# Optimization experiments

Measured on AMD Instinct MI355X. Metric: run time of the kernel, lower is better.

The kernel has to match this reference:

```python
import jax, jax.numpy as jnp
import numpy as np

D = 512       # input_embedding_dimensions
H = 2         # num_heads
HD = D // H   # head_dim = 256
B = 16
S = 1194      # max_sequence_length


def setup_inputs() -> dict:
    key = jax.random.key(0)
    k1, k2, k3, k4, k5 = jax.random.split(key, 5)
    scale_in = 1.0 / np.sqrt(D)
    return {
        "positional_embeddings": jax.random.normal(k1, (B, S, D), dtype=jnp.float32),
        "W_qkv": jax.random.uniform(k2, (D, 3 * D), minval=-scale_in, maxval=scale_in, dtype=jnp.float32),
        "b_qkv": jax.random.uniform(k3, (3 * D,), minval=-scale_in, maxval=scale_in, dtype=jnp.float32),
        "W_out": jax.random.uniform(k4, (D, D), minval=-scale_in, maxval=scale_in, dtype=jnp.float32),
        "b_out": jax.random.uniform(k5, (D,), minval=-scale_in, maxval=scale_in, dtype=jnp.float32),
    }


def reference(positional_embeddings, W_qkv, b_qkv, W_out, b_out):
    x = positional_embeddings              # [B, S, D]
    b, s, _ = x.shape
    qkv = x @ W_qkv + b_qkv                # [B, S, 3D]
    q, k, v = jnp.split(qkv, 3, axis=-1)

    def split_heads(t):
        return t.reshape(b, s, H, HD).transpose(0, 2, 1, 3)  # [B, H, S, HD]

    q, k, v = split_heads(q), split_heads(k), split_heads(v)
    scores = jnp.einsum("bhqd,bhkd->bhqk", q, k) / jnp.sqrt(jnp.float32(HD))
    causal = jnp.tril(jnp.ones((s, s), dtype=bool))          # [S, S]
    scores = jnp.where(causal[None, None, :, :], scores, -jnp.inf)
    att = jax.nn.softmax(scores, axis=-1)                    # [B, H, S, S]
    out = jnp.einsum("bhqk,bhkd->bhqd", att, v)              # [B, H, S, HD]
    out = out.transpose(0, 2, 1, 3).reshape(b, s, D)         # [B, S, D]
    return out @ W_out + b_out
```

## Files before the change

### kernel.cpp

```cpp
#include <hip/hip_runtime.h>
#include <stdint.h>

#define D_    512
#define H_    2
#define HD_   256
#define B_    16
#define S_    1194
#define MTOK  19104
#define MPAD  19200
#define SPAD  1216
#define NQKV  1536
#define NKT   38
#define LOG2E 1.44269504088896340736f

typedef unsigned short u16;
typedef __attribute__((ext_vector_type(8))) short bf16x8;
typedef __attribute__((ext_vector_type(4))) float f32x4;

__device__ inline u16 f2bf(float x) {
  union { float f; unsigned u; } c; c.f = x;
  unsigned r = c.u + 0x7fffu + ((c.u >> 16) & 1u);
  return (u16)(r >> 16);
}

__device__ inline void async_copy16(void* lds, const void* g) {
  __builtin_amdgcn_global_load_lds(
      (__attribute__((address_space(1))) void*)(g),
      (__attribute__((address_space(3))) void*)(lds),
      16, 0, 0);
}

__global__ void convert_kernel(const float* __restrict__ X,
                               const float* __restrict__ Wqkv,
                               const float* __restrict__ Wout,
                               u16* __restrict__ Xf,
                               u16* __restrict__ Wqf,
                               u16* __restrict__ Wof) {
  const int NXG = MPAD * 64;
  const int NQG = 12 * 8 * 16 * 64;
  const int NOG = 4 * 8 * 16 * 64;
  const int TOT = NXG + NQG + NOG;
  int stride = gridDim.x * blockDim.x;
  for (int g = blockIdx.x * blockDim.x + threadIdx.x; g < TOT; g += stride) {
    if (g < NXG) {
      int lane = g & 63, f = (g >> 6) & 15, kt = (g >> 10) & 7, mt = g >> 13;
      int i = mt * 128 + (f & 7) * 16 + (lane & 15);
      int k = kt * 64 + (f >> 3) * 32 + (lane >> 4) * 8;
      bf16x8 o;
      if (i < MTOK) {
        f32x4 v0 = *(const f32x4*)&X[(size_t)i * 512 + k];
        f32x4 v1 = *(const f32x4*)&X[(size_t)i * 512 + k + 4];
#pragma unroll
        for (int e = 0; e < 4; ++e) { o[e] = (short)f2bf(v0[e]); o[4 + e] = (short)f2bf(v1[e]); }
      } else {
#pragma unroll
        for (int e = 0; e < 8; ++e) o[e] = 0;
      }
      *(bf16x8*)&Xf[(size_t)g * 8] = o;
    } else if (g < NXG + NQG) {
      int gg = g - NXG;
      int lane = gg & 63, f = (gg >> 6) & 15, kt = (gg >> 10) & 7, nt = gg >> 13;
      int j = nt * 128 + (f & 7) * 16 + (lane & 15);
      int k = kt * 64 + (f >> 3) * 32 + (lane >> 4) * 8;
      bf16x8 o;
#pragma unroll
      for (int e = 0; e < 8; ++e) o[e] = (short)f2bf(Wqkv[(size_t)(k + e) * NQKV + j]);
      *(bf16x8*)&Wqf[(size_t)gg * 8] = o;
    } else {
      int gg = g - NXG - NQG;
      int lane = gg & 63, f = (gg >> 6) & 15, kt = (gg >> 10) & 7, nt = gg >> 13;
      int j = nt * 128 + (f & 7) * 16 + (lane & 15);
      int k = kt * 64 + (f >> 3) * 32 + (lane >> 4) * 8;
      bf16x8 o;
#pragma unroll
      for (int e = 0; e < 8; ++e) o[e] = (short)f2bf(Wout[(size_t)(k + e) * 512 + j]);
      *(bf16x8*)&Wof[(size_t)gg * 8] = o;
    }
  }
}

template<int MODE>
__global__ __launch_bounds__(256, 2) void gemm_kernel(
    const u16* __restrict__ Af, const u16* __restrict__ Bf,
    const float* __restrict__ bias, int nb,
    u16* __restrict__ Qb, u16* __restrict__ Kf, u16* __restrict__ Vf,
    float* __restrict__ Cout)
{
  __shared__ u16 ldsA[2][16 * 512];
  __shared__ u16 ldsB[2][16 * 512];

  const int t  = threadIdx.x;
  const int l  = t & 63;
  const int w  = t >> 6;
  const int lr = l >> 4, lc = l & 15;

  const int nwg = gridDim.x;
  const int qq = nwg >> 3, rr8 = nwg & 7;
  const int xcd = blockIdx.x & 7, off = blockIdx.x >> 3;
  const int wgid = (xcd < rr8 ? xcd * (qq + 1) : rr8 * (qq + 1) + (xcd - rr8) * qq) + off;
  const int m0 = (wgid / nb) * 128;
  const int n0 = (wgid % nb) * 128;

  const u16* pA = Af + ((size_t)(m0 >> 7) * 128 + w) * 512 + l * 8;
  const u16* pB = Bf + ((size_t)(n0 >> 7) * 128 + w) * 512 + l * 8;

  f32x4 acc[4][4] = {};

#pragma unroll
  for (int c = 0; c < 4; ++c) {
    async_copy16(&ldsA[0][(c * 4 + w) * 512], pA + c * 2048);
    async_copy16(&ldsB[0][(c * 4 + w) * 512], pB + c * 2048);
  }
  __syncthreads();

  for (int kt = 0; kt < 8; ++kt) {
    const int cur = kt & 1;
    if (kt < 7) {
      const u16* qA = pA + (kt + 1) * 8192;
      const u16* qB = pB + (kt + 1) * 8192;
#pragma unroll
      for (int c = 0; c < 4; ++c) {
        async_copy16(&ldsA[cur ^ 1][(c * 4 + w) * 512], qA + c * 2048);
        async_copy16(&ldsB[cur ^ 1][(c * 4 + w) * 512], qB + c * 2048);
      }
    }
#pragma unroll
    for (int kk = 0; kk < 2; ++kk) {
      bf16x8 af[4], bfr[4];
#pragma unroll
      for (int m = 0; m < 4; ++m)
        af[m] = *(bf16x8*)&ldsA[cur][((kk * 8 + (w >> 1) * 4 + m) * 64 + l) * 8];
#pragma unroll
      for (int n = 0; n < 4; ++n)
        bfr[n] = *(bf16x8*)&ldsB[cur][((kk * 8 + (w & 1) * 4 + n) * 64 + l) * 8];
      __builtin_amdgcn_s_setprio(1);
#pragma unroll
      for (int m = 0; m < 4; ++m)
#pragma unroll
        for (int n = 0; n < 4; ++n)
          acc[m][n] = __builtin_amdgcn_mfma_f32_16x16x32_bf16(af[m], bfr[n], acc[m][n], 0, 0, 0);
      __builtin_amdgcn_s_setprio(0);
    }
    __syncthreads();
  }

  int jv[4]; float bj[4];
#pragma unroll
  for (int n = 0; n < 4; ++n) { jv[n] = n0 + (w & 1) * 64 + n * 16 + lc; bj[n] = bias[jv[n]]; }

#pragma unroll
  for (int m = 0; m < 4; ++m) {
#pragma unroll
    for (int r = 0; r < 4; ++r) {
      int i = m0 + (w >> 1) * 64 + m * 16 + lr * 4 + r;
      if (i >= MTOK) continue;
      if (MODE == 0) {
        int b = i / S_, s = i - b * S_;
        int stK  = s >> 5;
        int nfs  = (s >> 4) & 1;
        int lisK = s & 15;
        int lvhi = (s >> 3) & 3;
        int es   = s & 7;
#pragma unroll
        for (int n = 0; n < 4; ++n) {
          int j = jv[n];
          int which = j >> 9, h = (j >> 8) & 1, d = j & 255;
          int bh = b * H_ + h;
          u16 v = f2bf(acc[m][n][r] + bj[n]);
          if (which == 0) {
            Qb[((size_t)(bh * SPAD + s)) * HD_ + d] = v;
          } else if (which == 1) {
            Kf[(((size_t)(bh * NKT + stK)) * 16 + (d >> 5) * 2 + nfs) * 512 +
               (((d >> 3) & 3) * 16 + lisK) * 8 + (d & 7)] = v;
          } else {
            Vf[(((size_t)(bh * NKT + stK)) * 16 + (d >> 4)) * 512 +
               (lvhi * 16 + (d & 15)) * 8 + es] = v;
          }
        }
      } else {
#pragma unroll
        for (int n = 0; n < 4; ++n)
          Cout[(size_t)i * D_ + jv[n]] = acc[m][n][r] + bj[n];
      }
    }
  }
}

__global__ __launch_bounds__(256, 2) void attn_kernel(
    const u16* __restrict__ Qb, const u16* __restrict__ Kf,
    const u16* __restrict__ Vf, u16* __restrict__ Obf)
{
  __shared__ u16 ldsK[2][16 * 512];
  __shared__ u16 ldsV[2][16 * 512];
  __shared__ u16 ldsP[4][16 * 36];

  const int id   = blockIdx.x;
  const int xcd  = id & 7;
  const int slot = id >> 3;
  const int bh   = xcd + 8 * (slot / 19);
  const int qt   = 18 - (slot % 19);
  const int q0   = qt * 64;
  const int nkv  = 2 * qt + 2;
  const int t  = threadIdx.x, l = t & 63, w = t >> 6;
  const int lr = l >> 4, lc = l & 15;
  const int wq0 = q0 + w * 16;

  bf16x8 qf[8];
  const u16* qbase = Qb + (size_t)(bh * SPAD + wq0 + lc) * HD_ + lr * 8;
#pragma unroll
  for (int kb = 0; kb < 8; ++kb)
    qf[kb] = *(const bf16x8*)(qbase + kb * 32);

  f32x4 oacc[16] = {};
  float mrow[4] = {-1e30f, -1e30f, -1e30f, -1e30f};
  float lsum[4] = {0.f, 0.f, 0.f, 0.f};

  {
    const u16* kb_ = Kf + (((size_t)(bh * NKT)) * 16 + w) * 512 + l * 8;
    const u16* vb_ = Vf + (((size_t)(bh * NKT)) * 16 + w) * 512 + l * 8;
#pragma unroll
    for (int c = 0; c < 4; ++c) {
      async_copy16(&ldsK[0][(c * 4 + w) * 512], kb_ + c * 2048);
      async_copy16(&ldsV[0][(c * 4 + w) * 512], vb_ + c * 2048);
    }
  }
  __syncthreads();

  for (int kt = 0; kt < nkv; ++kt) {
    const int cur = kt & 1;
    if (kt + 1 < nkv) {
      const u16* kb_ = Kf + (((size_t)(bh * NKT + kt + 1)) * 16 + w) * 512 + l * 8;
      const u16* vb_ = Vf + (((size_t)(bh * NKT + kt + 1)) * 16 + w) * 512 + l * 8;
#pragma unroll
      for (int c = 0; c < 4; ++c) {
        async_copy16(&ldsK[cur ^ 1][(c * 4 + w) * 512], kb_ + c * 2048);
        async_copy16(&ldsV[cur ^ 1][(c * 4 + w) * 512], vb_ + c * 2048);
      }
    }

    f32x4 sacc[2] = {};
    __builtin_amdgcn_s_setprio(1);
#pragma unroll
    for (int kb = 0; kb < 8; ++kb) {
#pragma unroll
      for (int nf = 0; nf < 2; ++nf) {
        bf16x8 kf = *(bf16x8*)&ldsK[cur][((kb * 2 + nf) * 64 + l) * 8];
        sacc[nf] = __builtin_amdgcn_mfma_f32_16x16x32_bf16(qf[kb], kf, sacc[nf], 0, 0, 0);
      }
    }
    __builtin_amdgcn_s_setprio(0);

    const int kv0 = kt * 32;
    float sval[2][4];
    float pm[4] = {-1e30f, -1e30f, -1e30f, -1e30f};
    if (kv0 + 31 <= wq0) {
#pragma unroll
      for (int nf = 0; nf < 2; ++nf)
#pragma unroll
        for (int r = 0; r < 4; ++r) {
          float v = sacc[nf][r] * 0.0625f;
          sval[nf][r] = v;
          pm[r] = fmaxf(pm[r], v);
        }
    } else {
#pragma unroll
      for (int nf = 0; nf < 2; ++nf) {
        int col = kv0 + nf * 16 + lc;
#pragma unroll
        for (int r = 0; r < 4; ++r) {
          int row = wq0 + lr * 4 + r;
          float v = ((col <= row) && (col < S_)) ? sacc[nf][r] * 0.0625f : -1e30f;
          sval[nf][r] = v;
          pm[r] = fmaxf(pm[r], v);
        }
      }
    }
#pragma unroll
    for (int r = 0; r < 4; ++r) {
      pm[r] = fmaxf(pm[r], __shfl_xor(pm[r], 1));
      pm[r] = fmaxf(pm[r], __shfl_xor(pm[r], 2));
      pm[r] = fmaxf(pm[r], __shfl_xor(pm[r], 4));
      pm[r] = fmaxf(pm[r], __shfl_xor(pm[r], 8));
    }
    bool skip = (pm[0] <= mrow[0] + 8.0f) && (pm[1] <= mrow[1] + 8.0f) &&
                (pm[2] <= mrow[2] + 8.0f) && (pm[3] <= mrow[3] + 8.0f);
    if (!__all(skip)) {
#pragma unroll
      for (int r = 0; r < 4; ++r) {
        float mn = fmaxf(mrow[r], pm[r]);
        float sc = exp2f((mrow[r] - mn) * LOG2E);
        mrow[r] = mn;
        lsum[r] *= sc;
#pragma unroll
        for (int nf = 0; nf < 16; ++nf) oacc[nf][r] *= sc;
      }
    }
#pragma unroll
    for (int nf = 0; nf < 2; ++nf)
#pragma unroll
      for (int r = 0; r < 4; ++r) {
        float p = exp2f((sval[nf][r] - mrow[r]) * LOG2E);
        lsum[r] += p;
        ldsP[w][(lr * 4 + r) * 36 + nf * 16 + lc] = f2bf(p);
      }

    bf16x8 pf = *(bf16x8*)&ldsP[w][lc * 36 + lr * 8];
    __builtin_amdgcn_s_setprio(1);
#pragma unroll
    for (int nf = 0; nf < 16; ++nf) {
      bf16x8 vf = *(bf16x8*)&ldsV[cur][(nf * 64 + l) * 8];
      oacc[nf] = __builtin_amdgcn_mfma_f32_16x16x32_bf16(pf, vf, oacc[nf], 0, 0, 0);
    }
    __builtin_amdgcn_s_setprio(0);
    __syncthreads();
  }

  float inv[4];
#pragma unroll
  for (int r = 0; r < 4; ++r) {
    float s = lsum[r];
    s += __shfl_xor(s, 1); s += __shfl_xor(s, 2);
    s += __shfl_xor(s, 4); s += __shfl_xor(s, 8);
    inv[r] = 1.0f / s;
  }
  const int b = bh >> 1, h = bh & 1;
#pragma unroll
  for (int r = 0; r < 4; ++r) {
    int qrow = wq0 + lr * 4 + r;
    if (qrow < S_) {
      int i = b * S_ + qrow;
      int it = i >> 7, mf = (i >> 4) & 7, li = i & 15;
#pragma unroll
      for (int nf = 0; nf < 16; ++nf) {
        int j = h * HD_ + nf * 16 + lc;
        size_t addr = (((size_t)(it * 8 + (j >> 6))) * 16 + ((j >> 5) & 1) * 8 + mf) * 512 +
                      (((j >> 3) & 3) * 16 + li) * 8 + (j & 7);
        Obf[addr] = f2bf(oacc[nf][r] * inv[r]);
      }
    }
  }
}

extern "C" void kernel_launch(void* const* d_in, const int* in_sizes, int n_in,
                              void* d_out, int out_size, void* d_ws, size_t ws_size,
                              hipStream_t stream) {
  const float* X    = (const float*)d_in[0];
  const float* Wqkv = (const float*)d_in[1];
  const float* bqkv = (const float*)d_in[2];
  const float* Wout = (const float*)d_in[3];
  const float* bout = (const float*)d_in[4];
  float* out = (float*)d_out;

  char* ws = (char*)d_ws;
  u16* Xf  = (u16*)ws;  ws += (size_t)MPAD * D_ * 2;
  u16* Wqf = (u16*)ws;  ws += (size_t)NQKV * D_ * 2;
  u16* Wof = (u16*)ws;  ws += (size_t)D_ * D_ * 2;
  u16* Qb  = (u16*)ws;  ws += (size_t)B_ * H_ * SPAD * HD_ * 2;
  u16* Kf  = (u16*)ws;  ws += (size_t)B_ * H_ * SPAD * HD_ * 2;
  u16* Vf  = (u16*)ws;  ws += (size_t)B_ * H_ * SPAD * HD_ * 2;
  u16* Obf = (u16*)ws;  ws += (size_t)MPAD * D_ * 2;

  convert_kernel<<<2048, 256, 0, stream>>>(X, Wqkv, Wout, Xf, Wqf, Wof);
  gemm_kernel<0><<<1800, 256, 0, stream>>>(Xf, Wqf, bqkv, 12, Qb, Kf, Vf, nullptr);
  attn_kernel<<<608, 256, 0, stream>>>(Qb, Kf, Vf, Obf);
  gemm_kernel<1><<<600, 256, 0, stream>>>(Obf, Wof, bout, 4, nullptr, nullptr, nullptr, out);
}
```

Measured before the change: 177.0 us.

## Process two 16-row query tiles per wave to double K/V reuse in attention

```diff
diff --git a/kernel.cpp b/kernel.cpp
--- a/kernel.cpp
+++ b/kernel.cpp
@@ -192,28 +192,35 @@
 {
   __shared__ u16 ldsK[2][16 * 512];
   __shared__ u16 ldsV[2][16 * 512];
-  __shared__ u16 ldsP[4][16 * 36];
+  __shared__ u16 ldsP[4][32 * 36];
 
   const int id   = blockIdx.x;
   const int xcd  = id & 7;
   const int slot = id >> 3;
-  const int bh   = xcd + 8 * (slot / 19);
-  const int qt   = 18 - (slot % 19);
-  const int q0   = qt * 64;
-  const int nkv  = 2 * qt + 2;
+  const int bh   = xcd + 8 * (slot / 10);
+  const int qt   = 9 - (slot % 10);
+  const int q0   = qt * 128;
+  const int nkv  = min(4 * qt + 4, NKT);
   const int t  = threadIdx.x, l = t & 63, w = t >> 6;
   const int lr = l >> 4, lc = l & 15;
-  const int wq0 = q0 + w * 16;
-
-  bf16x8 qf[8];
-  const u16* qbase = Qb + (size_t)(bh * SPAD + wq0 + lc) * HD_ + lr * 8;
-#pragma unroll
-  for (int kb = 0; kb < 8; ++kb)
-    qf[kb] = *(const bf16x8*)(qbase + kb * 32);
-
-  f32x4 oacc[16] = {};
-  float mrow[4] = {-1e30f, -1e30f, -1e30f, -1e30f};
-  float lsum[4] = {0.f, 0.f, 0.f, 0.f};
+  const int wq0 = q0 + w * 32;
+
+  bf16x8 qf[2][8];
+#pragma unroll
+  for (int a = 0; a < 2; ++a) {
+    int qr = wq0 + a * 16 + lc; if (qr >= S_) qr = S_ - 1;
+    const u16* qbase = Qb + (size_t)(bh * SPAD + qr) * HD_ + lr * 8;
+#pragma unroll
+    for (int kb = 0; kb < 8; ++kb)
+      qf[a][kb] = *(const bf16x8*)(qbase + kb * 32);
+  }
+
+  f32x4 oacc[2][16] = {};
+  float mrow[2][4], lsum[2][4];
+#pragma unroll
+  for (int a = 0; a < 2; ++a)
+#pragma unroll
+    for (int r = 0; r < 4; ++r) { mrow[a][r] = -1e30f; lsum[a][r] = 0.f; }
 
   {
     const u16* kb_ = Kf + (((size_t)(bh * NKT)) * 16 + w) * 512 + l * 8;
@@ -238,104 +245,122 @@
       }
     }
 
-    f32x4 sacc[2] = {};
+    f32x4 sacc[2][2] = {};
     __builtin_amdgcn_s_setprio(1);
 #pragma unroll
     for (int kb = 0; kb < 8; ++kb) {
 #pragma unroll
       for (int nf = 0; nf < 2; ++nf) {
         bf16x8 kf = *(bf16x8*)&ldsK[cur][((kb * 2 + nf) * 64 + l) * 8];
-        sacc[nf] = __builtin_amdgcn_mfma_f32_16x16x32_bf16(qf[kb], kf, sacc[nf], 0, 0, 0);
+        sacc[0][nf] = __builtin_amdgcn_mfma_f32_16x16x32_bf16(qf[0][kb], kf, sacc[0][nf], 0, 0, 0);
+        sacc[1][nf] = __builtin_amdgcn_mfma_f32_16x16x32_bf16(qf[1][kb], kf, sacc[1][nf], 0, 0, 0);
       }
     }
     __builtin_amdgcn_s_setprio(0);
 
     const int kv0 = kt * 32;
-    float sval[2][4];
-    float pm[4] = {-1e30f, -1e30f, -1e30f, -1e30f};
-    if (kv0 + 31 <= wq0) {
+    float pm[2][4];
+    float sval[2][2][4];
+#pragma unroll
+    for (int a = 0; a < 2; ++a) {
+#pragma unroll
+      for (int r = 0; r < 4; ++r) pm[a][r] = -1e30f;
+      if (kv0 + 31 <= wq0 + a * 16) {
+#pragma unroll
+        for (int nf = 0; nf < 2; ++nf)
+#pragma unroll
+          for (int r = 0; r < 4; ++r) {
+            float v = sacc[a][nf][r] * 0.0625f;
+            sval[a][nf][r] = v;
+            pm[a][r] = fmaxf(pm[a][r], v);
+          }
+      } else {
+#pragma unroll
+        for (int nf = 0; nf < 2; ++nf) {
+          int col = kv0 + nf * 16 + lc;
+#pragma unroll
+          for (int r = 0; r < 4; ++r) {
+            int row = wq0 + a * 16 + lr * 4 + r;
+            float v = ((col <= row) && (col < S_)) ? sacc[a][nf][r] * 0.0625f : -1e30f;
+            sval[a][nf][r] = v;
+            pm[a][r] = fmaxf(pm[a][r], v);
+          }
+        }
+      }
+#pragma unroll
+      for (int r = 0; r < 4; ++r) {
+        pm[a][r] = fmaxf(pm[a][r], __shfl_xor(pm[a][r], 1));
+        pm[a][r] = fmaxf(pm[a][r], __shfl_xor(pm[a][r], 2));
+        pm[a][r] = fmaxf(pm[a][r], __shfl_xor(pm[a][r], 4));
+        pm[a][r] = fmaxf(pm[a][r], __shfl_xor(pm[a][r], 8));
+      }
+    }
+    bool skip = true;
+#pragma unroll
+    for (int a = 0; a < 2; ++a)
+#pragma unroll
+      for (int r = 0; r < 4; ++r) skip = skip && (pm[a][r] <= mrow[a][r] + 8.0f);
+    if (!__all(skip)) {
+#pragma unroll
+      for (int a = 0; a < 2; ++a)
+#pragma unroll
+        for (int r = 0; r < 4; ++r) {
+          float mn = fmaxf(mrow[a][r], pm[a][r]);
+          float sc = exp2f((mrow[a][r] - mn) * LOG2E);
+          mrow[a][r] = mn;
+          lsum[a][r] *= sc;
+#pragma unroll
+          for (int nf = 0; nf < 16; ++nf) oacc[a][nf][r] *= sc;
+        }
+    }
+#pragma unroll
+    for (int a = 0; a < 2; ++a)
 #pragma unroll
       for (int nf = 0; nf < 2; ++nf)
 #pragma unroll
         for (int r = 0; r < 4; ++r) {
-          float v = sacc[nf][r] * 0.0625f;
-          sval[nf][r] = v;
-          pm[r] = fmaxf(pm[r], v);
-        }
-    } else {
-#pragma unroll
-      for (int nf = 0; nf < 2; ++nf) {
-        int col = kv0 + nf * 16 + lc;
-#pragma unroll
-        for (int r = 0; r < 4; ++r) {
-          int row = wq0 + lr * 4 + r;
-          float v = ((col <= row) && (col < S_)) ? sacc[nf][r] * 0.0625f : -1e30f;
-          sval[nf][r] = v;
-          pm[r] = fmaxf(pm[r], v);
-        }
-      }
-    }
-#pragma unroll
-    for (int r = 0; r < 4; ++r) {
-      pm[r] = fmaxf(pm[r], __shfl_xor(pm[r], 1));
-      pm[r] = fmaxf(pm[r], __shfl_xor(pm[r], 2));
-      pm[r] = fmaxf(pm[r], __shfl_xor(pm[r], 4));
-      pm[r] = fmaxf(pm[r], __shfl_xor(pm[r], 8));
-    }
-    bool skip = (pm[0] <= mrow[0] + 8.0f) && (pm[1] <= mrow[1] + 8.0f) &&
-                (pm[2] <= mrow[2] + 8.0f) && (pm[3] <= mrow[3] + 8.0f);
-    if (!__all(skip)) {
-#pragma unroll
-      for (int r = 0; r < 4; ++r) {
-        float mn = fmaxf(mrow[r], pm[r]);
-        float sc = exp2f((mrow[r] - mn) * LOG2E);
-        mrow[r] = mn;
-        lsum[r] *= sc;
-#pragma unroll
-        for (int nf = 0; nf < 16; ++nf) oacc[nf][r] *= sc;
-      }
-    }
-#pragma unroll
-    for (int nf = 0; nf < 2; ++nf)
-#pragma unroll
-      for (int r = 0; r < 4; ++r) {
-        float p = exp2f((sval[nf][r] - mrow[r]) * LOG2E);
-        lsum[r] += p;
-        ldsP[w][(lr * 4 + r) * 36 + nf * 16 + lc] = f2bf(p);
-      }
-
-    bf16x8 pf = *(bf16x8*)&ldsP[w][lc * 36 + lr * 8];
+          float p = exp2f((sval[a][nf][r] - mrow[a][r]) * LOG2E);
+          lsum[a][r] += p;
+          ldsP[w][(a * 16 + lr * 4 + r) * 36 + nf * 16 + lc] = f2bf(p);
+        }
+
+    bf16x8 pf0 = *(bf16x8*)&ldsP[w][lc * 36 + lr * 8];
+    bf16x8 pf1 = *(bf16x8*)&ldsP[w][(16 + lc) * 36 + lr * 8];
     __builtin_amdgcn_s_setprio(1);
 #pragma unroll
     for (int nf = 0; nf < 16; ++nf) {
       bf16x8 vf = *(bf16x8*)&ldsV[cur][(nf * 64 + l) * 8];
-      oacc[nf] = __builtin_amdgcn_mfma_f32_16x16x32_bf16(pf, vf, oacc[nf], 0, 0, 0);
+      oacc[0][nf] = __builtin_amdgcn_mfma_f32_16x16x32_bf16(pf0, vf, oacc[0][nf], 0, 0, 0);
+      oacc[1][nf] = __builtin_amdgcn_mfma_f32_16x16x32_bf16(pf1, vf, oacc[1][nf], 0, 0, 0);
     }
     __builtin_amdgcn_s_setprio(0);
     __syncthreads();
   }
 
-  float inv[4];
-#pragma unroll
-  for (int r = 0; r < 4; ++r) {
-    float s = lsum[r];
-    s += __shfl_xor(s, 1); s += __shfl_xor(s, 2);
-    s += __shfl_xor(s, 4); s += __shfl_xor(s, 8);
-    inv[r] = 1.0f / s;
-  }
   const int b = bh >> 1, h = bh & 1;
 #pragma unroll
-  for (int r = 0; r < 4; ++r) {
-    int qrow = wq0 + lr * 4 + r;
-    if (qrow < S_) {
-      int i = b * S_ + qrow;
-      int it = i >> 7, mf = (i >> 4) & 7, li = i & 15;
-#pragma unroll
-      for (int nf = 0; nf < 16; ++nf) {
-        int j = h * HD_ + nf * 16 + lc;
-        size_t addr = (((size_t)(it * 8 + (j >> 6))) * 16 + ((j >> 5) & 1) * 8 + mf) * 512 +
-                      (((j >> 3) & 3) * 16 + li) * 8 + (j & 7);
-        Obf[addr] = f2bf(oacc[nf][r] * inv[r]);
+  for (int a = 0; a < 2; ++a) {
+    float inv[4];
+#pragma unroll
+    for (int r = 0; r < 4; ++r) {
+      float s = lsum[a][r];
+      s += __shfl_xor(s, 1); s += __shfl_xor(s, 2);
+      s += __shfl_xor(s, 4); s += __shfl_xor(s, 8);
+      inv[r] = 1.0f / s;
+    }
+#pragma unroll
+    for (int r = 0; r < 4; ++r) {
+      int qrow = wq0 + a * 16 + lr * 4 + r;
+      if (qrow < S_) {
+        int i = b * S_ + qrow;
+        int it = i >> 7, mf = (i >> 4) & 7, li = i & 15;
+#pragma unroll
+        for (int nf = 0; nf < 16; ++nf) {
+          int j = h * HD_ + nf * 16 + lc;
+          size_t addr = (((size_t)(it * 8 + (j >> 6))) * 16 + ((j >> 5) & 1) * 8 + mf) * 512 +
+                        (((j >> 3) & 3) * 16 + li) * 8 + (j & 7);
+          Obf[addr] = f2bf(oacc[a][nf][r] * inv[r]);
+        }
       }
     }
   }
@@ -362,6 +387,6 @@
 
   convert_kernel<<<2048, 256, 0, stream>>>(X, Wqkv, Wout, Xf, Wqf, Wof);
   gemm_kernel<0><<<1800, 256, 0, stream>>>(Xf, Wqf, bqkv, 12, Qb, Kf, Vf, nullptr);
-  attn_kernel<<<608, 256, 0, stream>>>(Qb, Kf, Vf, Obf);
+  attn_kernel<<<320, 256, 0, stream>>>(Qb, Kf, Vf, Obf);
   gemm_kernel<1><<<600, 256, 0, stream>>>(Obf, Wof, bout, 4, nullptr, nullptr, nullptr, out);
 }
```

After: 226.4 us. +27.9%, slower.
